# Kernel tuning notes

Measured on AMD Instinct MI355X. Metric: run time of the kernel, lower is better.

## Reference

```python
import jax, jax.numpy as jnp
import numpy as np


def setup_inputs() -> dict:
    key = jax.random.key(0)
    ks = jax.random.split(key, 8)
    B, K, L, D = 8, 8, 4096, 256
    S = 1024  # windowlen
    inp = {
        "input": jax.random.normal(ks[0], (B, K, L, D), dtype=jnp.float32),
        "event_time": jax.random.uniform(ks[1], (B, L), dtype=jnp.float32),
        "W1": jax.random.normal(ks[2], (D, 2 * D), dtype=jnp.float32) / np.sqrt(D),
        "b1": jnp.zeros((2 * D,), dtype=jnp.float32),
        "W2": jax.random.normal(ks[3], (2 * D, D), dtype=jnp.float32) / np.sqrt(2 * D),
        "b2": jnp.zeros((D,), dtype=jnp.float32),
        "W3": jax.random.normal(ks[4], (D, 1), dtype=jnp.float32) / np.sqrt(D),
        "windowlen": S,
    }
    return inp


def reference(input, event_time, W1, b1, W2, b2, W3, windowlen):
    B, K, L, D = input.shape
    S = windowlen
    idx = jnp.arange(0, 2 * S, 2)  # strided window indices, [S]
    x = input.reshape(B * K, L, D)  # (BK, L, D)
    x_s = x[:, idx, :]  # (BK, S, D) indexed gather

    # offset MLP: D -> 2D -> D -> 1 (dropout inactive at eval)
    h = jax.nn.relu(jnp.einsum('bsd,de->bse', x_s, W1) + b1)
    h = jax.nn.relu(jnp.einsum('bse,ed->bsd', h, W2) + b2)
    offset = jnp.einsum('bsd,do->bso', h, W3)  # (BK, S, 1)

    pos = idx.astype(input.dtype)[None, :, None] + offset  # (BK, S, 1)

    # mask: pos <= argmax(event_time) per batch
    limit = jax.lax.stop_gradient(jnp.argmax(event_time, axis=-1)).astype(input.dtype)  # (B,)
    mask = (pos.reshape(B, K, S) <= limit[:, None, None]).astype(jnp.float32)  # (B, K, S)

    # grid x = pos/(L-1)*2-1 un-normalizes back to exactly pos; y=0 hits row 0.
    p = pos[..., 0]  # (BK, S)
    x0 = jnp.floor(p)
    w = p - x0  # fractional weight (grad flows to p, floor is constant)
    i0 = x0.astype(jnp.int32)
    i1 = i0 + 1

    def gather(i):
        valid = ((i >= 0) & (i <= L - 1)).astype(x.dtype)[..., None]
        ic = jnp.clip(i, 0, L - 1)
        return jnp.take_along_axis(x, ic[..., None], axis=1) * valid  # (BK, S, D)

    out = (1.0 - w)[..., None] * gather(i0) + w[..., None] * gather(i1)
    out = out.reshape(B, K, S, D)
    return out, mask
```

## Files before the change

### kernel.cpp

```cpp
#include <hip/hip_runtime.h>
#include <math.h>

#define B_   8
#define K_   8
#define L_   4096
#define D_   256
#define H_   512
#define S_   1024
#define M_   65536
#define MAXF 4096

typedef _Float16 half8  __attribute__((ext_vector_type(8)));
typedef float    floatx4 __attribute__((ext_vector_type(4)));

#define WS_LIMIT   0
#define WS_COUNTER 64
#define WS_FLAGS   128
#define WS_W1T     65536
#define WS_W2T     (65536 + H_*D_*2)

#define XA_LD    264
#define H1_LD    520
#define BS_LD    40
#define BS_ELEMS (256 * BS_LD)

__global__ __launch_bounds__(256) void prep_kernel(const float* __restrict__ et,
                                                   const float* __restrict__ W1,
                                                   const float* __restrict__ W2,
                                                   char* __restrict__ ws) {
  __shared__ float sv[256];
  __shared__ int   si[256];
  const int blk = blockIdx.x;
  const int t   = threadIdx.x;
  if (blk < 1024) {
    int e = blk * 256 + t;
    if (e < H_ * D_) {
      int n = e >> 8, k = e & 255;
      ((_Float16*)(ws + WS_W1T))[e] = (_Float16)W1[(size_t)k * H_ + n];
    } else {
      int e2 = e - H_ * D_;
      int n = e2 >> 9, k = e2 & 511;
      ((_Float16*)(ws + WS_W2T))[e2] = (_Float16)W2[(size_t)k * D_ + n];
    }
  } else if (blk < 1032) {
    int b = blk - 1024;
    const float* row = et + (size_t)b * L_;
    float best = -INFINITY; int bidx = 0;
    for (int i = t; i < L_; i += 256) {
      float v = row[i];
      if (v > best) { best = v; bidx = i; }
    }
    sv[t] = best; si[t] = bidx;
    __syncthreads();
    for (int sft = 128; sft > 0; sft >>= 1) {
      if (t < sft) {
        float v2 = sv[t + sft]; int i2 = si[t + sft];
        if (v2 > sv[t] || (v2 == sv[t] && i2 < si[t])) { sv[t] = v2; si[t] = i2; }
      }
      __syncthreads();
    }
    if (t == 0) ((float*)(ws + WS_LIMIT))[b] = (float)si[0];
  } else {
    if (t == 0) *(int*)(ws + WS_COUNTER) = 0;
  }
}

__device__ __forceinline__ void run_gemm(
    const _Float16* __restrict__ Bglob, const int ldb, const int nsteps,
    const _Float16* __restrict__ Alds, const int lda,
    _Float16* __restrict__ Bs, const int t, floatx4 (&acc)[2][8])
{
  const int lane = t & 63, w = t >> 6;
  const int lr = lane & 15, quad = lane >> 4;
  const int rowoff = (w & 1) * 32, coloff = (w >> 1) * 128;
  const int sr = lane >> 2, sk = lane & 3;
  const int srow0 = w * 64 + sr;

  uint4 breg[4];
  #pragma unroll
  for (int c = 0; c < 4; ++c)
    breg[c] = *(const uint4*)(Bglob + (size_t)(srow0 + c * 16) * ldb + sk * 8);
  #pragma unroll
  for (int c = 0; c < 4; ++c)
    *(uint4*)((char*)Bs + (srow0 + c * 16) * (BS_LD * 2) + sk * 16) = breg[c];
  __syncthreads();

  for (int ks = 0; ks < nsteps; ++ks) {
    const _Float16* Bcur = Bs + (ks & 1) * BS_ELEMS;
    if (ks + 1 < nsteps) {
      const _Float16* src = Bglob + (ks + 1) * 32 + sk * 8;
      #pragma unroll
      for (int c = 0; c < 4; ++c)
        breg[c] = *(const uint4*)(src + (size_t)(srow0 + c * 16) * ldb);
    }
    half8 af[2], bf[8];
    #pragma unroll
    for (int mt = 0; mt < 2; ++mt)
      af[mt] = *(const half8*)(Alds + (rowoff + mt * 16 + lr) * lda + ks * 32 + quad * 8);
    #pragma unroll
    for (int nt = 0; nt < 8; ++nt)
      bf[nt] = *(const half8*)(Bcur + (coloff + nt * 16 + lr) * BS_LD + quad * 8);
    #pragma unroll
    for (int mt = 0; mt < 2; ++mt)
      #pragma unroll
      for (int nt = 0; nt < 8; ++nt)
        acc[mt][nt] = __builtin_amdgcn_mfma_f32_16x16x32_f16(af[mt], bf[nt], acc[mt][nt], 0, 0, 0);
    if (ks + 1 < nsteps) {
      _Float16* Bnxt = Bs + ((ks + 1) & 1) * BS_ELEMS;
      #pragma unroll
      for (int c = 0; c < 4; ++c)
        *(uint4*)((char*)Bnxt + (srow0 + c * 16) * (BS_LD * 2) + sk * 16) = breg[c];
    }
    __syncthreads();
  }
}

__global__ __launch_bounds__(256, 1) void fused_kernel(
    const float* __restrict__ X, char* __restrict__ ws,
    const float* __restrict__ b1, const float* __restrict__ b2,
    const float* __restrict__ W3,
    float* __restrict__ out, float* __restrict__ maskv) {
  __shared__ __align__(16) _Float16 Xa[64 * XA_LD];
  __shared__ __align__(16) _Float16 h1s[64 * H1_LD];
  __shared__ __align__(16) _Float16 Bs[2 * BS_ELEMS];
  __shared__ float psum[2][64];
  __shared__ float posl[64];

  const _Float16* W1T    = (const _Float16*)(ws + WS_W1T);
  const _Float16* W2T    = (const _Float16*)(ws + WS_W2T);
  const float*    limitf = (const float*)(ws + WS_LIMIT);
  int*            counter = (int*)(ws + WS_COUNTER);
  int*            flags   = (int*)(ws + WS_FLAGS);

  const int t    = threadIdx.x;
  const int m0   = blockIdx.x * 64;
  const int lane = t & 63, w = t >> 6;
  const int lr   = lane & 15, quad = lane >> 4;
  const int rowoff = (w & 1) * 32, coloff = (w >> 1) * 128;
  const int bk   = m0 >> 10;

  {
    const int r = t >> 2, q = t & 3;
    const int s = (m0 + r) & 1023;
    const float* xrow = X + ((size_t)bk * L_ + 2 * s) * D_ + q * 64;
    _Float16* dst = Xa + r * XA_LD + q * 64;
    #pragma unroll
    for (int i = 0; i < 8; ++i) {
      float4 v0 = *(const float4*)(xrow + i * 8);
      float4 v1 = *(const float4*)(xrow + i * 8 + 4);
      half8 h;
      h[0]=(_Float16)v0.x; h[1]=(_Float16)v0.y; h[2]=(_Float16)v0.z; h[3]=(_Float16)v0.w;
      h[4]=(_Float16)v1.x; h[5]=(_Float16)v1.y; h[6]=(_Float16)v1.z; h[7]=(_Float16)v1.w;
      *(half8*)(dst + i * 8) = h;
    }
  }

  floatx4 acc[2][8];

  #pragma unroll
  for (int nh = 0; nh < 2; ++nh) {
    #pragma unroll
    for (int mt = 0; mt < 2; ++mt)
      #pragma unroll
      for (int nt = 0; nt < 8; ++nt)
        acc[mt][nt] = (floatx4){0.f, 0.f, 0.f, 0.f};
    run_gemm(W1T + (size_t)nh * 256 * D_, D_, 8, Xa, XA_LD, Bs, t, acc);
    #pragma unroll
    for (int nt = 0; nt < 8; ++nt) {
      int col = nh * 256 + coloff + nt * 16 + lr;
      float bias = b1[col];
      #pragma unroll
      for (int mt = 0; mt < 2; ++mt) {
        int rowb = rowoff + mt * 16 + quad * 4;
        #pragma unroll
        for (int rg = 0; rg < 4; ++rg) {
          float v = acc[mt][nt][rg] + bias;
          h1s[(rowb + rg) * H1_LD + col] = (_Float16)(v > 0.f ? v : 0.f);
        }
      }
    }
  }

  #pragma unroll
  for (int mt = 0; mt < 2; ++mt)
    #pragma unroll
    for (int nt = 0; nt < 8; ++nt)
      acc[mt][nt] = (floatx4){0.f, 0.f, 0.f, 0.f};
  run_gemm(W2T, H_, 16, h1s, H1_LD, Bs, t, acc);

  float part[2][4] = {{0,0,0,0},{0,0,0,0}};
  #pragma unroll
  for (int nt = 0; nt < 8; ++nt) {
    int col = coloff + nt * 16 + lr;
    float bias = b2[col];
    float w3   = W3[col];
    #pragma unroll
    for (int mt = 0; mt < 2; ++mt)
      #pragma unroll
      for (int rg = 0; rg < 4; ++rg) {
        float h2 = acc[mt][nt][rg] + bias;
        h2 = h2 > 0.f ? h2 : 0.f;
        part[mt][rg] = fmaf(h2, w3, part[mt][rg]);
      }
  }
  #pragma unroll
  for (int mt = 0; mt < 2; ++mt)
    #pragma unroll
    for (int rg = 0; rg < 4; ++rg) {
      float p = part[mt][rg];
      p += __shfl_xor(p, 1, 64);
      p += __shfl_xor(p, 2, 64);
      p += __shfl_xor(p, 4, 64);
      p += __shfl_xor(p, 8, 64);
      if (lr == 0) psum[w >> 1][rowoff + mt * 16 + quad * 4 + rg] = p;
    }
  __syncthreads();
  if (t < 64) {
    int   mrow  = m0 + t;
    float off   = psum[0][t] + psum[1][t];
    int   s     = mrow & 1023;
    float pos   = (float)(2 * s) + off;
    float limit = limitf[mrow >> 13];
    maskv[mrow] = (pos <= limit) ? 1.f : 0.f;
    posl[t] = pos;
    float d = pos - limit;
    if (d < 0.5f && d > -0.5f) {
      int idx = atomicAdd(counter, 1);
      if (idx < MAXF) flags[idx] = mrow;
    }
  }
  __syncthreads();
  {
    const int c4 = t & 63, rg = t >> 6;
    const float* xbase = X + (size_t)bk * (L_ * D_);
    #pragma unroll 4
    for (int rr = 0; rr < 16; ++rr) {
      int   rI = rg * 16 + rr;
      float p  = posl[rI];
      float x0f = floorf(p);
      float ww  = p - x0f;
      int i0 = (int)x0f, i1 = i0 + 1;
      float v0 = (i0 >= 0 && i0 < L_) ? (1.f - ww) : 0.f;
      float v1 = (i1 >= 0 && i1 < L_) ? ww : 0.f;
      int ic0 = min(max(i0, 0), L_ - 1), ic1 = min(max(i1, 0), L_ - 1);
      float4 g0 = *(const float4*)(xbase + (size_t)ic0 * D_ + c4 * 4);
      float4 g1 = *(const float4*)(xbase + (size_t)ic1 * D_ + c4 * 4);
      float4 o;
      o.x = v0 * g0.x + v1 * g1.x;
      o.y = v0 * g0.y + v1 * g1.y;
      o.z = v0 * g0.z + v1 * g1.z;
      o.w = v0 * g0.w + v1 * g1.w;
      *(float4*)(out + (size_t)(m0 + rI) * D_ + c4 * 4) = o;
    }
  }
}

__global__ __launch_bounds__(256) void fixup_kernel(
    const float* __restrict__ X,  const float* __restrict__ W1,
    const float* __restrict__ b1, const float* __restrict__ W2,
    const float* __restrict__ b2, const float* __restrict__ W3,
    const char* __restrict__ ws, float* __restrict__ maskv) {
  __shared__ float xs[256];
  __shared__ float h1f[512];
  __shared__ float red[4];
  const float* limitf  = (const float*)(ws + WS_LIMIT);
  const int*   counter = (const int*)(ws + WS_COUNTER);
  const int*   flags   = (const int*)(ws + WS_FLAGS);
  const int t = threadIdx.x;
  const int cnt = min(*counter, MAXF);
  for (int fi = blockIdx.x; fi < cnt; fi += 64) {
    int mrow = flags[fi];
    int bk = mrow >> 10, s = mrow & 1023;
    const float* xrow = X + ((size_t)bk * L_ + 2 * s) * D_;
    xs[t] = xrow[t];
    __syncthreads();
    #pragma unroll
    for (int jj = 0; jj < 2; ++jj) {
      int j = t + jj * 256;
      float a = b1[j];
      for (int d = 0; d < 256; ++d)
        a = fmaf(xs[d], W1[(size_t)d * H_ + j], a);
      h1f[j] = a > 0.f ? a : 0.f;
    }
    __syncthreads();
    {
      float a = b2[t];
      for (int e = 0; e < 512; ++e)
        a = fmaf(h1f[e], W2[(size_t)e * D_ + t], a);
      float h2 = a > 0.f ? a : 0.f;
      float pp = h2 * W3[t];
      #pragma unroll
      for (int o = 32; o >= 1; o >>= 1) pp += __shfl_xor(pp, o, 64);
      if ((t & 63) == 0) red[t >> 6] = pp;
    }
    __syncthreads();
    if (t == 0) {
      float off   = red[0] + red[1] + red[2] + red[3];
      float pos   = (float)(2 * s) + off;
      float limit = limitf[mrow >> 13];
      maskv[mrow] = (pos <= limit) ? 1.f : 0.f;
    }
    __syncthreads();
  }
}

extern "C" void kernel_launch(void* const* d_in, const int* in_sizes, int n_in,
                              void* d_out, int out_size, void* d_ws, size_t ws_size,
                              hipStream_t stream) {
  const float* X  = (const float*)d_in[0];
  const float* et = (const float*)d_in[1];
  const float* W1 = (const float*)d_in[2];
  const float* b1 = (const float*)d_in[3];
  const float* W2 = (const float*)d_in[4];
  const float* b2 = (const float*)d_in[5];
  const float* W3 = (const float*)d_in[6];
  float* out   = (float*)d_out;
  float* maskv = out + (size_t)M_ * D_;
  char*  ws    = (char*)d_ws;

  prep_kernel <<<1033, 256, 0, stream>>>(et, W1, W2, ws);
  fused_kernel<<<1024, 256, 0, stream>>>(X, ws, b1, b2, W3, out, maskv);
  fixup_kernel<<<64,   256, 0, stream>>>(X, W1, b1, W2, b2, W3, ws, maskv);
}
```

Baseline: 482.3 us.

## Halve fused-kernel row tile to 32 and single-buffer B tile for higher occupancy

Each fused block now handles 32 rows instead of 64. The four waves split the N dimension 64 columns each, and partial W3 dot products are reduced across four waves. The B staging buffer drops from double to single buffering with an extra barrier per k-step, and the launch_bounds minimum-blocks hint is removed. Together these cut LDS and register use so more blocks fit per CU. In exchange, each block re-streams the same weights over half as many rows, roughly doubling weight traffic, and pays more synchronisation.

Measured after the change: 660.4 us. +36.9%, slower.

```diff
diff --git a/kernel.cpp b/kernel.cpp
--- a/kernel.cpp
+++ b/kernel.cpp
@@ -22,7 +22,6 @@
 #define XA_LD    264
 #define H1_LD    520
 #define BS_LD    40
-#define BS_ELEMS (256 * BS_LD)
 
 __global__ __launch_bounds__(256) void prep_kernel(const float* __restrict__ et,
                                                    const float* __restrict__ W1,
@@ -68,11 +67,11 @@
 __device__ __forceinline__ void run_gemm(
     const _Float16* __restrict__ Bglob, const int ldb, const int nsteps,
     const _Float16* __restrict__ Alds, const int lda,
-    _Float16* __restrict__ Bs, const int t, floatx4 (&acc)[2][8])
+    _Float16* __restrict__ Bs, const int t, floatx4 (&acc)[2][4])
 {
   const int lane = t & 63, w = t >> 6;
   const int lr = lane & 15, quad = lane >> 4;
-  const int rowoff = (w & 1) * 32, coloff = (w >> 1) * 128;
+  const int coloff = w * 64;
   const int sr = lane >> 2, sk = lane & 3;
   const int srow0 = w * 64 + sr;
 
@@ -83,48 +82,46 @@
   #pragma unroll
   for (int c = 0; c < 4; ++c)
     *(uint4*)((char*)Bs + (srow0 + c * 16) * (BS_LD * 2) + sk * 16) = breg[c];
-  __syncthreads();
 
   for (int ks = 0; ks < nsteps; ++ks) {
-    const _Float16* Bcur = Bs + (ks & 1) * BS_ELEMS;
+    __syncthreads();
     if (ks + 1 < nsteps) {
       const _Float16* src = Bglob + (ks + 1) * 32 + sk * 8;
       #pragma unroll
       for (int c = 0; c < 4; ++c)
         breg[c] = *(const uint4*)(src + (size_t)(srow0 + c * 16) * ldb);
     }
-    half8 af[2], bf[8];
+    half8 af[2], bf[4];
     #pragma unroll
     for (int mt = 0; mt < 2; ++mt)
-      af[mt] = *(const half8*)(Alds + (rowoff + mt * 16 + lr) * lda + ks * 32 + quad * 8);
-    #pragma unroll
-    for (int nt = 0; nt < 8; ++nt)
-      bf[nt] = *(const half8*)(Bcur + (coloff + nt * 16 + lr) * BS_LD + quad * 8);
+      af[mt] = *(const half8*)(Alds + (mt * 16 + lr) * lda + ks * 32 + quad * 8);
+    #pragma unroll
+    for (int nt = 0; nt < 4; ++nt)
+      bf[nt] = *(const half8*)(Bs + (coloff + nt * 16 + lr) * BS_LD + quad * 8);
     #pragma unroll
     for (int mt = 0; mt < 2; ++mt)
       #pragma unroll
-      for (int nt = 0; nt < 8; ++nt)
+      for (int nt = 0; nt < 4; ++nt)
         acc[mt][nt] = __builtin_amdgcn_mfma_f32_16x16x32_f16(af[mt], bf[nt], acc[mt][nt], 0, 0, 0);
+    __syncthreads();
     if (ks + 1 < nsteps) {
-      _Float16* Bnxt = Bs + ((ks + 1) & 1) * BS_ELEMS;
       #pragma unroll
       for (int c = 0; c < 4; ++c)
-        *(uint4*)((char*)Bnxt + (srow0 + c * 16) * (BS_LD * 2) + sk * 16) = breg[c];
-    }
-    __syncthreads();
-  }
-}
-
-__global__ __launch_bounds__(256, 1) void fused_kernel(
+        *(uint4*)((char*)Bs + (srow0 + c * 16) * (BS_LD * 2) + sk * 16) = breg[c];
+    }
+  }
+}
+
+__global__ __launch_bounds__(256) void fused_kernel(
     const float* __restrict__ X, char* __restrict__ ws,
     const float* __restrict__ b1, const float* __restrict__ b2,
     const float* __restrict__ W3,
     float* __restrict__ out, float* __restrict__ maskv) {
-  __shared__ __align__(16) _Float16 Xa[64 * XA_LD];
-  __shared__ __align__(16) _Float16 h1s[64 * H1_LD];
-  __shared__ __align__(16) _Float16 Bs[2 * BS_ELEMS];
-  __shared__ float psum[2][64];
-  __shared__ float posl[64];
+  __shared__ __align__(16) _Float16 Xa[32 * XA_LD];
+  __shared__ __align__(16) _Float16 h1s[32 * H1_LD];
+  __shared__ __align__(16) _Float16 Bs[256 * BS_LD];
+  __shared__ float psum[4][32];
+  __shared__ float posl[32];
 
   const _Float16* W1T    = (const _Float16*)(ws + WS_W1T);
   const _Float16* W2T    = (const _Float16*)(ws + WS_W2T);
@@ -133,19 +130,18 @@
   int*            flags   = (int*)(ws + WS_FLAGS);
 
   const int t    = threadIdx.x;
-  const int m0   = blockIdx.x * 64;
+  const int m0   = blockIdx.x * 32;
   const int lane = t & 63, w = t >> 6;
   const int lr   = lane & 15, quad = lane >> 4;
-  const int rowoff = (w & 1) * 32, coloff = (w >> 1) * 128;
   const int bk   = m0 >> 10;
 
   {
-    const int r = t >> 2, q = t & 3;
+    const int r = t >> 3, q = t & 7;
     const int s = (m0 + r) & 1023;
-    const float* xrow = X + ((size_t)bk * L_ + 2 * s) * D_ + q * 64;
-    _Float16* dst = Xa + r * XA_LD + q * 64;
-    #pragma unroll
-    for (int i = 0; i < 8; ++i) {
+    const float* xrow = X + ((size_t)bk * L_ + 2 * s) * D_ + q * 32;
+    _Float16* dst = Xa + r * XA_LD + q * 32;
+    #pragma unroll
+    for (int i = 0; i < 4; ++i) {
       float4 v0 = *(const float4*)(xrow + i * 8);
       float4 v1 = *(const float4*)(xrow + i * 8 + 4);
       half8 h;
@@ -155,23 +151,23 @@
     }
   }
 
-  floatx4 acc[2][8];
+  floatx4 acc[2][4];
 
   #pragma unroll
   for (int nh = 0; nh < 2; ++nh) {
     #pragma unroll
     for (int mt = 0; mt < 2; ++mt)
       #pragma unroll
-      for (int nt = 0; nt < 8; ++nt)
+      for (int nt = 0; nt < 4; ++nt)
         acc[mt][nt] = (floatx4){0.f, 0.f, 0.f, 0.f};
     run_gemm(W1T + (size_t)nh * 256 * D_, D_, 8, Xa, XA_LD, Bs, t, acc);
     #pragma unroll
-    for (int nt = 0; nt < 8; ++nt) {
-      int col = nh * 256 + coloff + nt * 16 + lr;
+    for (int nt = 0; nt < 4; ++nt) {
+      int col = nh * 256 + w * 64 + nt * 16 + lr;
       float bias = b1[col];
       #pragma unroll
       for (int mt = 0; mt < 2; ++mt) {
-        int rowb = rowoff + mt * 16 + quad * 4;
+        int rowb = mt * 16 + quad * 4;
         #pragma unroll
         for (int rg = 0; rg < 4; ++rg) {
           float v = acc[mt][nt][rg] + bias;
@@ -184,14 +180,14 @@
   #pragma unroll
   for (int mt = 0; mt < 2; ++mt)
     #pragma unroll
-    for (int nt = 0; nt < 8; ++nt)
+    for (int nt = 0; nt < 4; ++nt)
       acc[mt][nt] = (floatx4){0.f, 0.f, 0.f, 0.f};
   run_gemm(W2T, H_, 16, h1s, H1_LD, Bs, t, acc);
 
   float part[2][4] = {{0,0,0,0},{0,0,0,0}};
   #pragma unroll
-  for (int nt = 0; nt < 8; ++nt) {
-    int col = coloff + nt * 16 + lr;
+  for (int nt = 0; nt < 4; ++nt) {
+    int col = w * 64 + nt * 16 + lr;
     float bias = b2[col];
     float w3   = W3[col];
     #pragma unroll
@@ -212,12 +208,12 @@
       p += __shfl_xor(p, 2, 64);
       p += __shfl_xor(p, 4, 64);
       p += __shfl_xor(p, 8, 64);
-      if (lr == 0) psum[w >> 1][rowoff + mt * 16 + quad * 4 + rg] = p;
+      if (lr == 0) psum[w][mt * 16 + quad * 4 + rg] = p;
     }
   __syncthreads();
-  if (t < 64) {
+  if (t < 32) {
     int   mrow  = m0 + t;
-    float off   = psum[0][t] + psum[1][t];
+    float off   = psum[0][t] + psum[1][t] + psum[2][t] + psum[3][t];
     int   s     = mrow & 1023;
     float pos   = (float)(2 * s) + off;
     float limit = limitf[mrow >> 13];
@@ -231,11 +227,11 @@
   }
   __syncthreads();
   {
-    const int c4 = t & 63, rg = t >> 6;
+    const int c4 = t & 63, rgp = t >> 6;
     const float* xbase = X + (size_t)bk * (L_ * D_);
     #pragma unroll 4
-    for (int rr = 0; rr < 16; ++rr) {
-      int   rI = rg * 16 + rr;
+    for (int rr = 0; rr < 8; ++rr) {
+      int   rI = rgp * 8 + rr;
       float p  = posl[rI];
       float x0f = floorf(p);
       float ww  = p - x0f;
@@ -319,6 +315,6 @@
   char*  ws    = (char*)d_ws;
 
   prep_kernel <<<1033, 256, 0, stream>>>(et, W1, W2, ws);
-  fused_kernel<<<1024, 256, 0, stream>>>(X, ws, b1, b2, W3, out, maskv);
+  fused_kernel<<<2048, 256, 0, stream>>>(X, ws, b1, b2, W3, out, maskv);
   fixup_kernel<<<64,   256, 0, stream>>>(X, W1, b1, W2, b2, W3, ws, maskv);
 }
```
